# Kernel optimization log

Hardware: AMD Instinct MI355X
Metric: run time of the kernel (lower is better)

Reference implementation:

```python
import jax, jax.numpy as jnp
import numpy as np

N_ENT = 100000   # entities per KG
N_EDGE = 500000  # edges per KG
N_SEED = 10000
DIM = 128


def _norm_adj(edges, n):
    # edges: [E,2] int. Build undirected adjacency + self loops, sym deg^-1/2 norm.
    loop = jnp.arange(n)
    src = jnp.concatenate([edges[:, 0], edges[:, 1], loop])
    dst = jnp.concatenate([edges[:, 1], edges[:, 0], loop])
    deg = jax.ops.segment_sum(jnp.ones(src.shape[0], jnp.float32), dst, num_segments=n)
    norm = jax.lax.rsqrt(deg[src] * deg[dst])  # [E_tot]
    return src, dst, norm


def _gcn(x, edges, Ws, n):
    # MultiLayerGCN: per layer H = relu(A_norm @ X @ W + X) (residual=True)
    src, dst, norm = _norm_adj(edges, n)
    for W in Ws:
        agg = jax.ops.segment_sum(x[src] * norm[:, None], dst, num_segments=n)  # [n,d]
        x = jax.nn.relu(agg @ W + x)
    return x


def setup_inputs() -> dict:
    key = jax.random.key(0)
    ks = jax.random.split(key, 10)
    return {
        "sr_ent_seeds": jax.random.randint(ks[0], (N_SEED,), 0, N_ENT),
        "tg_ent_seeds": jax.random.randint(ks[1], (N_SEED,), 0, N_ENT),
        "triples_sr": jax.random.randint(ks[2], (N_EDGE, 3), 0, N_ENT),
        "triples_tg": jax.random.randint(ks[3], (N_EDGE, 3), 0, N_ENT),
        "embedding_sr": jax.random.normal(ks[4], (N_ENT, DIM), jnp.float32),
        "embedding_tg": jax.random.normal(ks[5], (N_ENT, DIM), jnp.float32),
        "edges_sr": jax.random.randint(ks[6], (N_EDGE, 2), 0, N_ENT),
        "edges_tg": jax.random.randint(ks[7], (N_EDGE, 2), 0, N_ENT),
        "W1": jax.random.normal(ks[8], (DIM, DIM), jnp.float32) * (DIM ** -0.5),
        "W2": jax.random.normal(ks[9], (DIM, DIM), jnp.float32) * (DIM ** -0.5),
    }


def reference(sr_ent_seeds, tg_ent_seeds, triples_sr, triples_tg,
              embedding_sr, embedding_tg, edges_sr, edges_tg, W1, W2):
    Ws = [W1, W2]
    sr_ent_hid = _gcn(embedding_sr, edges_sr, Ws, N_ENT)
    tg_ent_hid = _gcn(embedding_tg, edges_tg, Ws, N_ENT)
    sr_seed_hid = sr_ent_hid[sr_ent_seeds]
    tg_seed_hid = tg_ent_hid[tg_ent_seeds]
    return (sr_seed_hid, tg_seed_hid, sr_ent_hid, tg_ent_hid)
```

## Files before the change

### kernel.cpp

```cpp
#include <hip/hip_runtime.h>
#include <hip/hip_bf16.h>

#define N_ENT_C   100000
#define N_EDGE_C  500000
#define N_SEED_C  10000
#define DIM_C     128

#define N2_C      (2 * N_ENT_C)
#define NBKT      391
#define BKT_CAP   8192
#define EPB       2048

typedef unsigned int   u32;
typedef unsigned short u16;
typedef __attribute__((ext_vector_type(8))) short bf16x8;
typedef __attribute__((ext_vector_type(4))) float f32x4;

__device__ __forceinline__ float bflo(u32 v) { return __uint_as_float(v << 16); }
__device__ __forceinline__ float bfhi(u32 v) { return __uint_as_float(v & 0xFFFF0000u); }
__device__ __forceinline__ u16 f2bf(float f) {
  u32 u = __float_as_uint(f);
  u += 0x7FFFu + ((u >> 16) & 1u);
  return (u16)(u >> 16);
}

__global__ void k_detect(const u32* __restrict__ words, int* __restrict__ flag,
                         int* __restrict__ bkt_cnt) {
  int tid = threadIdx.x;
  bkt_cnt[tid] = 0;
  bkt_cnt[tid + 256] = 0;
  if (tid == 0) {
    int cnt = 0;
    for (int i = 0; i < 64; ++i) {
      u32 e = (words[i] >> 7) & 0xFF;
      cnt += (e < 96) ? 1 : 0;
    }
    *flag = (cnt >= 8) ? 1 : 0;
  }
}

__global__ __launch_bounds__(256, 4) void k_fill_binned(
    const int2* __restrict__ ea, const int2* __restrict__ eb,
    int* __restrict__ bkt_cnt, u32* __restrict__ csr_tmp, int E) {
  __shared__ u32 ein[2 * EPB];
  __shared__ u16 ebkt[2 * EPB];
  __shared__ int lcount[512];
  __shared__ int lstart[513];
  __shared__ int gbase[512];
  __shared__ int ssc[256];

  const int tid = threadIdx.x;
  const int gofs = blockIdx.y ? N_ENT_C : 0;
  const int2* ed = blockIdx.y ? eb : ea;
  const int e0 = blockIdx.x * EPB;

  lcount[tid] = 0; lcount[tid + 256] = 0;
  __syncthreads();

  int2 ev[EPB / 256];
#pragma unroll
  for (int i = 0; i < EPB / 256; ++i) {
    int e = e0 + tid + i * 256;
    int2 v = (e < E) ? ed[e] : make_int2(0, 0);
    ev[i] = v;
    if (e < E) {
      atomicAdd(&lcount[(gofs + v.y) >> 9], 1);
      atomicAdd(&lcount[(gofs + v.x) >> 9], 1);
    }
  }
  __syncthreads();

  int a = lcount[2 * tid], b = lcount[2 * tid + 1];
  int ts = a + b;
  ssc[tid] = ts;
  __syncthreads();
  for (int off = 1; off < 256; off <<= 1) {
    int v = (tid >= off) ? ssc[tid - off] : 0;
    __syncthreads();
    ssc[tid] += v;
    __syncthreads();
  }
  int ex = ssc[tid] - ts;
  lstart[2 * tid] = ex;
  lstart[2 * tid + 1] = ex + a;
  if (tid == 255) lstart[512] = ssc[255];
  __syncthreads();

  {
    int b0 = 2 * tid, b1 = 2 * tid + 1;
    if (b0 < NBKT) { int c = lstart[b0 + 1] - lstart[b0]; gbase[b0] = c ? atomicAdd(&bkt_cnt[b0], c) : 0; }
    if (b1 < NBKT) { int c = lstart[b1 + 1] - lstart[b1]; gbase[b1] = c ? atomicAdd(&bkt_cnt[b1], c) : 0; }
    lcount[tid] = lstart[tid];
    lcount[tid + 256] = lstart[tid + 256];
  }
  __syncthreads();

#pragma unroll
  for (int i = 0; i < EPB / 256; ++i) {
    int e = e0 + tid + i * 256;
    if (e >= E) continue;
    int2 v = ev[i];
    int r1 = gofs + v.y;
    u32 w1 = (u32)v.x | ((u32)(r1 & 511) << 20);
    int bk1 = r1 >> 9;
    int p = atomicAdd(&lcount[bk1], 1);
    ein[p] = w1; ebkt[p] = (u16)bk1;
    int r2 = gofs + v.x;
    u32 w2 = (u32)v.y | ((u32)(r2 & 511) << 20);
    int bk2 = r2 >> 9;
    p = atomicAdd(&lcount[bk2], 1);
    ein[p] = w2; ebkt[p] = (u16)bk2;
  }
  __syncthreads();

  int tot = lstart[512];
  for (int j = tid; j < tot; j += 256) {
    int bk = ebkt[j];
    u32 off = (u32)(gbase[bk] + (j - lstart[bk]));
    if (off < BKT_CAP) csr_tmp[(size_t)bk * BKT_CAP + off] = ein[j];
  }
}

__global__ void k_deg(const u32* __restrict__ csr_tmp, const int* __restrict__ bkt_cnt,
                      int* __restrict__ deg, float* __restrict__ rdeg) {
  __shared__ int lcnt[512];
  int bk = blockIdx.x, tid = threadIdx.x;
  lcnt[tid] = 0;
  __syncthreads();
  int cnt = min(bkt_cnt[bk], BKT_CAP);
  const u32* src = csr_tmp + (size_t)bk * BKT_CAP;
  for (int j = tid; j < cnt; j += 512)
    atomicAdd(&lcnt[(src[j] >> 20) & 511], 1);
  __syncthreads();
  int row = (bk << 9) + tid;
  if (row < N2_C) {
    int d = lcnt[tid];
    deg[row] = d;
    rdeg[row] = rsqrtf((float)(d + 1));
  }
}

__global__ void k_scan1(const int* __restrict__ deg, int* __restrict__ row_start,
                        int* __restrict__ bsum, int n) {
  __shared__ int s[256];
  int b = blockIdx.x, tid = threadIdx.x;
  int i0 = b * 1024 + tid * 4;
  int d0 = (i0 + 0 < n) ? deg[i0 + 0] : 0;
  int d1 = (i0 + 1 < n) ? deg[i0 + 1] : 0;
  int d2 = (i0 + 2 < n) ? deg[i0 + 2] : 0;
  int d3 = (i0 + 3 < n) ? deg[i0 + 3] : 0;
  int tsum = d0 + d1 + d2 + d3;
  s[tid] = tsum;
  __syncthreads();
  for (int off = 1; off < 256; off <<= 1) {
    int v = (tid >= off) ? s[tid - off] : 0;
    __syncthreads();
    s[tid] += v;
    __syncthreads();
  }
  int toff = s[tid] - tsum;
  if (i0 + 0 < n) row_start[i0 + 0] = toff;
  if (i0 + 1 < n) row_start[i0 + 1] = toff + d0;
  if (i0 + 2 < n) row_start[i0 + 2] = toff + d0 + d1;
  if (i0 + 3 < n) row_start[i0 + 3] = toff + d0 + d1 + d2;
  if (tid == 255) bsum[b] = s[255];
}

__global__ void k_scan2(int* __restrict__ bsum, int nb) {
  __shared__ int s[256];
  int tid = threadIdx.x;
  int v = (tid < nb) ? bsum[tid] : 0;
  s[tid] = v;
  __syncthreads();
  for (int off = 1; off < 256; off <<= 1) {
    int u = (tid >= off) ? s[tid - off] : 0;
    __syncthreads();
    s[tid] += u;
    __syncthreads();
  }
  if (tid < nb) bsum[tid] = s[tid] - v;
}

__global__ void k_scan3(int* __restrict__ row_start, const int* __restrict__ bsum, int n) {
  int i = blockIdx.x * 256 + threadIdx.x;
  if (i < n) row_start[i] += bsum[i >> 10];
}

__global__ void k_csr_sort(const u32* __restrict__ csr_tmp, const int* __restrict__ bkt_cnt,
                           const int* __restrict__ row_start, const float* __restrict__ rdeg,
                           int2* __restrict__ csr) {
  __shared__ int lcur[512];
  int bk = blockIdx.x, tid = threadIdx.x;
  int rb0 = bk << 9;
  int base = row_start[rb0];
  {
    int row = rb0 + tid;
    lcur[tid] = (row < N2_C) ? row_start[row] - base : 0;
  }
  __syncthreads();
  int cnt = min(bkt_cnt[bk], BKT_CAP);
  const u32* srcp = csr_tmp + (size_t)bk * BKT_CAP;
  for (int j = tid; j < cnt; j += 512) {
    u32 w = srcp[j];
    int dl = (w >> 20) & 511;
    int s = w & 0x1FFFF;
    int pos = atomicAdd(&lcur[dl], 1);
    float r = rdeg[((rb0 + dl) >= N_ENT_C ? N_ENT_C : 0) + s];
    csr[base + pos] = make_int2(s, __float_as_int(r));
  }
}

__global__ void k_cvt_bf16(const void* __restrict__ s0, const void* __restrict__ s1,
                           u32* __restrict__ d0, u32* __restrict__ d1,
                           const int* __restrict__ flag, int n4) {
  int i = blockIdx.x * 256 + threadIdx.x;
  if (i >= n4) return;
  const void* src = blockIdx.y ? s1 : s0;
  u32* dst = blockIdx.y ? d1 : d0;
  uint4 o;
  if (*flag) {
    const float4* sf = (const float4*)src;
    float4 va = sf[2 * i], vb = sf[2 * i + 1];
    o.x = (u32)f2bf(va.x) | ((u32)f2bf(va.y) << 16);
    o.y = (u32)f2bf(va.z) | ((u32)f2bf(va.w) << 16);
    o.z = (u32)f2bf(vb.x) | ((u32)f2bf(vb.y) << 16);
    o.w = (u32)f2bf(vb.z) | ((u32)f2bf(vb.w) << 16);
  } else {
    o = ((const uint4*)src)[i];
  }
  ((uint4*)dst)[i] = o;
}

#define G2(cp, t, a0, a1) { \
  int2 e0 = cp[t], e1 = cp[(t) + 1]; \
  u32 v0 = xin[((u32)e0.x << 6) | lane]; \
  u32 v1 = xin[((u32)e1.x << 6) | lane]; \
  float r0 = __int_as_float(e0.y), r1 = __int_as_float(e1.y); \
  a0 += r0 * bflo(v0) + r1 * bflo(v1); \
  a1 += r0 * bfhi(v0) + r1 * bfhi(v1); }
#define G1(cp, t, a0, a1) { \
  int2 e0 = cp[t]; \
  u32 v0 = xin[((u32)e0.x << 6) | lane]; \
  float r0 = __int_as_float(e0.y); \
  a0 += r0 * bflo(v0); a1 += r0 * bfhi(v0); }

__global__ __launch_bounds__(512, 8) void k_fused(
    const int* __restrict__ row_start, const int* __restrict__ deg,
    const int2* __restrict__ csr2, const u32* __restrict__ xin0,
    const u32* __restrict__ xin1, const float* __restrict__ rdeg,
    const void* __restrict__ W, const int* __restrict__ flag,
    u32* __restrict__ xout0, u32* __restrict__ xout1,
    float* __restrict__ fout0, float* __restrict__ fout1) {
  __shared__ __align__(16) u16 smem[128 * 128 + 32 * 128];
  u16* sWt = smem;
  u16* sA  = smem + 128 * 128;

  const int tid = threadIdx.x;
  const int row0 = blockIdx.x * 32;
  const int gofs = blockIdx.y * N_ENT_C;
  const u32* __restrict__ xin  = blockIdx.y ? xin1  : xin0;
  u32* __restrict__ xout       = blockIdx.y ? xout1 : xout0;
  float* __restrict__ fout     = blockIdx.y ? fout1 : fout0;
  const int* rsb = row_start + gofs;
  const int* dgb = deg + gofs;
  const float* rdb = rdeg + gofs;
  const int isf32 = *flag;

  {
    u32* sW32 = (u32*)sWt;
    const float* Wf = (const float*)W;
    const u16*   Wu = (const u16*)W;
    for (int i = tid; i < 64 * 128; i += 512) {
      int k2 = i >> 7;
      int n  = i & 127;
      u16 lo, hi;
      if (isf32) { lo = f2bf(Wf[(2 * k2) * 128 + n]); hi = f2bf(Wf[(2 * k2 + 1) * 128 + n]); }
      else       { lo = Wu[(2 * k2) * 128 + n];       hi = Wu[(2 * k2 + 1) * 128 + n]; }
      sW32[n * 64 + (k2 ^ ((n & 7) << 2))] = (u32)lo | ((u32)hi << 16);
    }
  }

  const int wave = tid >> 6, lane = tid & 63;
  for (int pq = 0; pq < 2; ++pq) {
    const int rlA = wave * 4 + 2 * pq, rlB = rlA + 1;
    const int rowA = row0 + rlA, rowB = row0 + rlB;
    const bool vA = rowA < N_ENT_C, vB = rowB < N_ENT_C;
    int rsA = vA ? rsb[rowA] : 0, deA = vA ? dgb[rowA] : 0;
    int rsB = vB ? rsb[rowB] : 0, deB = vB ? dgb[rowB] : 0;
    rsA = __builtin_amdgcn_readfirstlane(rsA); deA = __builtin_amdgcn_readfirstlane(deA);
    rsB = __builtin_amdgcn_readfirstlane(rsB); deB = __builtin_amdgcn_readfirstlane(deB);
    const float rdA = vA ? rdb[rowA] : 0.f, rdB = vB ? rdb[rowB] : 0.f;
    const u32 vsA = vA ? xin[((u32)rowA << 6) | lane] : 0u;
    const u32 vsB = vB ? xin[((u32)rowB << 6) | lane] : 0u;
    const int2* cA = csr2 + rsA;
    const int2* cB = csr2 + rsB;
    float a0A = 0.f, a1A = 0.f, a0B = 0.f, a1B = 0.f;
    int tA = 0, tB = 0;
    while (tA + 1 < deA && tB + 1 < deB) {
      int2 eA0 = cA[tA], eA1 = cA[tA + 1];
      int2 eB0 = cB[tB], eB1 = cB[tB + 1];
      u32 uA0 = xin[((u32)eA0.x << 6) | lane];
      u32 uA1 = xin[((u32)eA1.x << 6) | lane];
      u32 uB0 = xin[((u32)eB0.x << 6) | lane];
      u32 uB1 = xin[((u32)eB1.x << 6) | lane];
      float rA0 = __int_as_float(eA0.y), rA1 = __int_as_float(eA1.y);
      float rB0 = __int_as_float(eB0.y), rB1 = __int_as_float(eB1.y);
      a0A += rA0 * bflo(uA0) + rA1 * bflo(uA1);
      a1A += rA0 * bfhi(uA0) + rA1 * bfhi(uA1);
      a0B += rB0 * bflo(uB0) + rB1 * bflo(uB1);
      a1B += rB0 * bfhi(uB0) + rB1 * bfhi(uB1);
      tA += 2; tB += 2;
    }
    for (; tA + 3 < deA; tA += 4) { G2(cA, tA, a0A, a1A); G2(cA, tA + 2, a0A, a1A); }
    if (tA + 1 < deA) { G2(cA, tA, a0A, a1A); tA += 2; }
    if (tA < deA) G1(cA, tA, a0A, a1A);
    for (; tB + 3 < deB; tB += 4) { G2(cB, tB, a0B, a1B); G2(cB, tB + 2, a0B, a1B); }
    if (tB + 1 < deB) { G2(cB, tB, a0B, a1B); tB += 2; }
    if (tB < deB) G1(cB, tB, a0B, a1B);

    a0A = rdA * a0A + rdA * rdA * bflo(vsA);
    a1A = rdA * a1A + rdA * rdA * bfhi(vsA);
    a0B = rdB * a0B + rdB * rdB * bflo(vsB);
    a1B = rdB * a1B + rdB * rdB * bfhi(vsB);
    ((u32*)sA)[rlA * 64 + (lane ^ ((rlA & 7) << 2))] = (u32)f2bf(a0A) | ((u32)f2bf(a1A) << 16);
    ((u32*)sA)[rlB * 64 + (lane ^ ((rlB & 7) << 2))] = (u32)f2bf(a0B) | ((u32)f2bf(a1B) << 16);
  }
  __syncthreads();

  const int rows_h = (wave >> 2) * 16;
  const int col_q  = (wave & 3) * 32;
  const int m = lane & 15, q = lane >> 4;
  f32x4 acc[2];
  for (int ct = 0; ct < 2; ++ct) acc[ct] = (f32x4){0.f, 0.f, 0.f, 0.f};
#pragma unroll
  for (int kt = 0; kt < 4; ++kt) {
    int k0 = kt * 32 + q * 8;
    int ks = k0 ^ ((m & 7) << 3);
    bf16x8 a = *(const bf16x8*)&sA[(rows_h + m) * 128 + ks];
#pragma unroll
    for (int ct = 0; ct < 2; ++ct) {
      bf16x8 b = *(const bf16x8*)&sWt[(col_q + ct * 16 + m) * 128 + ks];
      acc[ct] = __builtin_amdgcn_mfma_f32_16x16x32_bf16(a, b, acc[ct], 0, 0, 0);
    }
  }
  __syncthreads();

  float* sC = (float*)smem;
#pragma unroll
  for (int ct = 0; ct < 2; ++ct)
#pragma unroll
    for (int r = 0; r < 4; ++r)
      sC[(rows_h + q * 4 + r) * 132 + (col_q + ct * 16 + m)] = acc[ct][r];
  __syncthreads();

  {
    int rowl = tid >> 4;
    int c0 = (tid & 15) * 8;
    int row = row0 + rowl;
    if (row < N_ENT_C) {
      size_t goff = (size_t)row * 64 + (c0 >> 1);
      const u32* resp = xin + goff;
      if (fout) {
        float* op = fout + (size_t)row * 128 + c0;
#pragma unroll
        for (int u2 = 0; u2 < 2; ++u2) {
          u32 rv0 = resp[2 * u2], rv1 = resp[2 * u2 + 1];
          f32x4 f;
          f[0] = fmaxf(sC[rowl * 132 + c0 + 4 * u2    ] + bflo(rv0), 0.f);
          f[1] = fmaxf(sC[rowl * 132 + c0 + 4 * u2 + 1] + bfhi(rv0), 0.f);
          f[2] = fmaxf(sC[rowl * 132 + c0 + 4 * u2 + 2] + bflo(rv1), 0.f);
          f[3] = fmaxf(sC[rowl * 132 + c0 + 4 * u2 + 3] + bfhi(rv1), 0.f);
          __builtin_nontemporal_store(f, (f32x4*)(op + 4 * u2));
        }
      } else {
        u32 ov[4];
#pragma unroll
        for (int u = 0; u < 4; ++u) {
          u32 rv = resp[u];
          float lo = fmaxf(sC[rowl * 132 + c0 + 2 * u]     + bflo(rv), 0.f);
          float hi = fmaxf(sC[rowl * 132 + c0 + 2 * u + 1] + bfhi(rv), 0.f);
          ov[u] = (u32)f2bf(lo) | ((u32)f2bf(hi) << 16);
        }
        uint4* op = (uint4*)(xout + goff);
        op[0] = make_uint4(ov[0], ov[1], ov[2], ov[3]);
      }
    }
  }
}

__global__ void k_out_seed(const float4* __restrict__ ea, const float4* __restrict__ eb,
                           const int* __restrict__ sa, const int* __restrict__ sb,
                           float4* __restrict__ oa, float4* __restrict__ ob, int total4) {
  int t = blockIdx.x * 256 + threadIdx.x;
  if (t >= total4) return;
  const float4* e = blockIdx.y ? eb : ea;
  const int* seeds = blockIdx.y ? sb : sa;
  float4* o = blockIdx.y ? ob : oa;
  int s = t >> 5, w = t & 31;
  o[t] = e[((size_t)seeds[s] << 5) | w];
}

extern "C" void kernel_launch(void* const* d_in, const int* in_sizes, int n_in,
                              void* d_out, int out_size, void* d_ws, size_t ws_size,
                              hipStream_t stream) {
  const int*  sr_seeds = (const int*)d_in[0];
  const int*  tg_seeds = (const int*)d_in[1];
  const void* emb_sr   = d_in[4];
  const void* emb_tg   = d_in[5];
  const int*  edges_sr = (const int*)d_in[6];
  const int*  edges_tg = (const int*)d_in[7];
  const void* W1       = d_in[8];
  const void* W2       = d_in[9];
  float* out = (float*)d_out;

  const int nd = N_ENT_C * DIM_C;

  u16* x_A       = (u16*)d_ws;
  u16* x_B       = x_A + (size_t)nd;
  float* ws_rdeg = (float*)(x_B + (size_t)nd);
  int* ws_flag   = (int*)(ws_rdeg + N2_C);
  int* deg       = ws_flag + 64;
  int* row_start = deg + N2_C;
  int* bsum      = row_start + N2_C;
  int* bkt_cnt   = bsum + 1024;
  int2* csr      = (int2*)(bkt_cnt + 512);
  u32* csr_tmp   = (u32*)(csr + (size_t)4 * N_EDGE_C);
  u16* x_C       = (u16*)csr_tmp;

  float* out_seed_sr = out;
  float* out_seed_tg = out + (size_t)N_SEED_C * DIM_C;
  float* out_ent_sr  = out + (size_t)2 * N_SEED_C * DIM_C;
  float* out_ent_tg  = out_ent_sr + (size_t)nd;

  u16* x_D = (u16*)out_ent_sr;

  k_detect<<<1, 256, 0, stream>>>((const u32*)emb_sr, ws_flag, bkt_cnt);

  dim3 agrid((N_EDGE_C + EPB - 1) / EPB, 2);
  k_fill_binned<<<agrid, 256, 0, stream>>>((const int2*)edges_sr, (const int2*)edges_tg,
                                           bkt_cnt, csr_tmp, N_EDGE_C);
  k_deg<<<NBKT, 512, 0, stream>>>(csr_tmp, bkt_cnt, deg, ws_rdeg);

  const int NB_SCAN = (N2_C + 1023) / 1024;
  k_scan1<<<NB_SCAN, 256, 0, stream>>>(deg, row_start, bsum, N2_C);
  k_scan2<<<1, 256, 0, stream>>>(bsum, NB_SCAN);
  k_scan3<<<(N2_C + 255) / 256, 256, 0, stream>>>(row_start, bsum, N2_C);

  k_csr_sort<<<NBKT, 512, 0, stream>>>(csr_tmp, bkt_cnt, row_start, ws_rdeg, csr);

  dim3 cgrid((nd / 8 + 255) / 256, 2);
  k_cvt_bf16<<<cgrid, 256, 0, stream>>>(emb_sr, emb_tg, (u32*)x_A, (u32*)x_B, ws_flag, nd / 8);

  const int NBF = N_ENT_C / 32;

  dim3 f2grid(NBF, 2);
  k_fused<<<f2grid, 512, 0, stream>>>(row_start, deg, csr, (const u32*)x_A, (const u32*)x_B,
                                      ws_rdeg, W1, ws_flag, (u32*)x_C, (u32*)x_D,
                                      nullptr, nullptr);

  k_fused<<<dim3(NBF, 1), 512, 0, stream>>>(row_start + N_ENT_C, deg + N_ENT_C, csr,
                                            (const u32*)x_D, nullptr, ws_rdeg + N_ENT_C,
                                            W2, ws_flag, nullptr, nullptr,
                                            out_ent_tg, nullptr);
  k_fused<<<dim3(NBF, 1), 512, 0, stream>>>(row_start, deg, csr,
                                            (const u32*)x_C, nullptr, ws_rdeg,
                                            W2, ws_flag, nullptr, nullptr,
                                            out_ent_sr, nullptr);

  dim3 sgrid((N_SEED_C * 32 + 255) / 256, 2);
  k_out_seed<<<sgrid, 256, 0, stream>>>((const float4*)out_ent_sr, (const float4*)out_ent_tg,
                                        sr_seeds, tg_seeds,
                                        (float4*)out_seed_sr, (float4*)out_seed_tg,
                                        N_SEED_C * 32);
}
```

Measured before the change: 523.9 us.

## Build CSR offsets per bucket and drop embedded edge weights from CSR

Replaces the three-pass global degree scan with a scan over bucket counts plus a per-bucket local scan inside the CSR sort, so the separate degree array and two kernel launches go away. CSR entries shrink from int2 (index plus rdeg) to a bare u32 index. The aggregation kernel now looks up rdeg by source index, and it derives degrees from adjacent row_start values. This removes the rdeg gather during the sort and halves CSR bandwidth, at the cost of an extra scalar-indexed rdeg load per edge in the hot loop. Row-validity guards are also removed, which relies on N_ENT being a multiple of 32.

After: 523.5 us. No clear change (-0.1%).

```diff
diff --git a/kernel.cpp b/kernel.cpp
--- a/kernel.cpp
+++ b/kernel.cpp
@@ -122,7 +122,7 @@
 }
 
 __global__ void k_deg(const u32* __restrict__ csr_tmp, const int* __restrict__ bkt_cnt,
-                      int* __restrict__ deg, float* __restrict__ rdeg) {
+                      float* __restrict__ rdeg) {
   __shared__ int lcnt[512];
   int bk = blockIdx.x, tid = threadIdx.x;
   lcnt[tid] = 0;
@@ -133,80 +133,60 @@
     atomicAdd(&lcnt[(src[j] >> 20) & 511], 1);
   __syncthreads();
   int row = (bk << 9) + tid;
-  if (row < N2_C) {
-    int d = lcnt[tid];
-    deg[row] = d;
-    rdeg[row] = rsqrtf((float)(d + 1));
-  }
-}
-
-__global__ void k_scan1(const int* __restrict__ deg, int* __restrict__ row_start,
-                        int* __restrict__ bsum, int n) {
-  __shared__ int s[256];
-  int b = blockIdx.x, tid = threadIdx.x;
-  int i0 = b * 1024 + tid * 4;
-  int d0 = (i0 + 0 < n) ? deg[i0 + 0] : 0;
-  int d1 = (i0 + 1 < n) ? deg[i0 + 1] : 0;
-  int d2 = (i0 + 2 < n) ? deg[i0 + 2] : 0;
-  int d3 = (i0 + 3 < n) ? deg[i0 + 3] : 0;
-  int tsum = d0 + d1 + d2 + d3;
-  s[tid] = tsum;
-  __syncthreads();
-  for (int off = 1; off < 256; off <<= 1) {
-    int v = (tid >= off) ? s[tid - off] : 0;
-    __syncthreads();
-    s[tid] += v;
-    __syncthreads();
-  }
-  int toff = s[tid] - tsum;
-  if (i0 + 0 < n) row_start[i0 + 0] = toff;
-  if (i0 + 1 < n) row_start[i0 + 1] = toff + d0;
-  if (i0 + 2 < n) row_start[i0 + 2] = toff + d0 + d1;
-  if (i0 + 3 < n) row_start[i0 + 3] = toff + d0 + d1 + d2;
-  if (tid == 255) bsum[b] = s[255];
-}
-
-__global__ void k_scan2(int* __restrict__ bsum, int nb) {
-  __shared__ int s[256];
+  if (row < N2_C) rdeg[row] = rsqrtf((float)(lcnt[tid] + 1));
+}
+
+__global__ void k_scanb(const int* __restrict__ bkt_cnt, int* __restrict__ bbase,
+                        int* __restrict__ row_start) {
+  __shared__ int s[512];
   int tid = threadIdx.x;
-  int v = (tid < nb) ? bsum[tid] : 0;
+  int v = (tid < NBKT) ? bkt_cnt[tid] : 0;
   s[tid] = v;
   __syncthreads();
-  for (int off = 1; off < 256; off <<= 1) {
+  for (int off = 1; off < 512; off <<= 1) {
     int u = (tid >= off) ? s[tid - off] : 0;
     __syncthreads();
     s[tid] += u;
     __syncthreads();
   }
-  if (tid < nb) bsum[tid] = s[tid] - v;
-}
-
-__global__ void k_scan3(int* __restrict__ row_start, const int* __restrict__ bsum, int n) {
-  int i = blockIdx.x * 256 + threadIdx.x;
-  if (i < n) row_start[i] += bsum[i >> 10];
-}
-
-__global__ void k_csr_sort(const u32* __restrict__ csr_tmp, const int* __restrict__ bkt_cnt,
-                           const int* __restrict__ row_start, const float* __restrict__ rdeg,
-                           int2* __restrict__ csr) {
-  __shared__ int lcur[512];
+  if (tid < NBKT) bbase[tid] = s[tid] - v;
+  if (tid == NBKT - 1) row_start[N2_C] = s[tid];
+}
+
+__global__ __launch_bounds__(512) void k_csr_sort(
+    const u32* __restrict__ csr_tmp, const int* __restrict__ bkt_cnt,
+    const int* __restrict__ bbase, int* __restrict__ row_start,
+    u32* __restrict__ csr) {
+  __shared__ int lcnt[512];
+  __shared__ int lofs[512];
   int bk = blockIdx.x, tid = threadIdx.x;
-  int rb0 = bk << 9;
-  int base = row_start[rb0];
-  {
-    int row = rb0 + tid;
-    lcur[tid] = (row < N2_C) ? row_start[row] - base : 0;
-  }
+  lcnt[tid] = 0;
   __syncthreads();
   int cnt = min(bkt_cnt[bk], BKT_CAP);
+  int base = bbase[bk];
   const u32* srcp = csr_tmp + (size_t)bk * BKT_CAP;
+  for (int j = tid; j < cnt; j += 512)
+    atomicAdd(&lcnt[(srcp[j] >> 20) & 511], 1);
+  __syncthreads();
+  int own = lcnt[tid];
+  lofs[tid] = own;
+  __syncthreads();
+  for (int off = 1; off < 512; off <<= 1) {
+    int u = (tid >= off) ? lofs[tid - off] : 0;
+    __syncthreads();
+    lofs[tid] += u;
+    __syncthreads();
+  }
+  int ex = lofs[tid] - own;
+  int row = (bk << 9) + tid;
+  if (row < N2_C) row_start[row] = base + ex;
+  lcnt[tid] = ex;
+  __syncthreads();
   for (int j = tid; j < cnt; j += 512) {
     u32 w = srcp[j];
     int dl = (w >> 20) & 511;
-    int s = w & 0x1FFFF;
-    int pos = atomicAdd(&lcur[dl], 1);
-    float r = rdeg[((rb0 + dl) >= N_ENT_C ? N_ENT_C : 0) + s];
-    csr[base + pos] = make_int2(s, __float_as_int(r));
+    int pos = atomicAdd(&lcnt[dl], 1);
+    csr[base + pos] = w & 0x1FFFF;
   }
 }
 
@@ -232,24 +212,24 @@
 }
 
 #define G2(cp, t, a0, a1) { \
-  int2 e0 = cp[t], e1 = cp[(t) + 1]; \
-  u32 v0 = xin[((u32)e0.x << 6) | lane]; \
-  u32 v1 = xin[((u32)e1.x << 6) | lane]; \
-  float r0 = __int_as_float(e0.y), r1 = __int_as_float(e1.y); \
+  u32 s0 = __builtin_amdgcn_readfirstlane(cp[t]); \
+  u32 s1 = __builtin_amdgcn_readfirstlane(cp[(t) + 1]); \
+  float r0 = rdb[s0], r1 = rdb[s1]; \
+  u32 v0 = xin[(s0 << 6) | lane]; \
+  u32 v1 = xin[(s1 << 6) | lane]; \
   a0 += r0 * bflo(v0) + r1 * bflo(v1); \
   a1 += r0 * bfhi(v0) + r1 * bfhi(v1); }
 #define G1(cp, t, a0, a1) { \
-  int2 e0 = cp[t]; \
-  u32 v0 = xin[((u32)e0.x << 6) | lane]; \
-  float r0 = __int_as_float(e0.y); \
+  u32 s0 = __builtin_amdgcn_readfirstlane(cp[t]); \
+  float r0 = rdb[s0]; \
+  u32 v0 = xin[(s0 << 6) | lane]; \
   a0 += r0 * bflo(v0); a1 += r0 * bfhi(v0); }
 
 __global__ __launch_bounds__(512, 8) void k_fused(
-    const int* __restrict__ row_start, const int* __restrict__ deg,
-    const int2* __restrict__ csr2, const u32* __restrict__ xin0,
-    const u32* __restrict__ xin1, const float* __restrict__ rdeg,
-    const void* __restrict__ W, const int* __restrict__ flag,
-    u32* __restrict__ xout0, u32* __restrict__ xout1,
+    const int* __restrict__ row_start, const u32* __restrict__ csru,
+    const u32* __restrict__ xin0, const u32* __restrict__ xin1,
+    const float* __restrict__ rdeg, const void* __restrict__ W,
+    const int* __restrict__ flag, u32* __restrict__ xout0, u32* __restrict__ xout1,
     float* __restrict__ fout0, float* __restrict__ fout1) {
   __shared__ __align__(16) u16 smem[128 * 128 + 32 * 128];
   u16* sWt = smem;
@@ -262,7 +242,6 @@
   u32* __restrict__ xout       = blockIdx.y ? xout1 : xout0;
   float* __restrict__ fout     = blockIdx.y ? fout1 : fout0;
   const int* rsb = row_start + gofs;
-  const int* dgb = deg + gofs;
   const float* rdb = rdeg + gofs;
   const int isf32 = *flag;
 
@@ -284,27 +263,28 @@
   for (int pq = 0; pq < 2; ++pq) {
     const int rlA = wave * 4 + 2 * pq, rlB = rlA + 1;
     const int rowA = row0 + rlA, rowB = row0 + rlB;
-    const bool vA = rowA < N_ENT_C, vB = rowB < N_ENT_C;
-    int rsA = vA ? rsb[rowA] : 0, deA = vA ? dgb[rowA] : 0;
-    int rsB = vB ? rsb[rowB] : 0, deB = vB ? dgb[rowB] : 0;
-    rsA = __builtin_amdgcn_readfirstlane(rsA); deA = __builtin_amdgcn_readfirstlane(deA);
-    rsB = __builtin_amdgcn_readfirstlane(rsB); deB = __builtin_amdgcn_readfirstlane(deB);
-    const float rdA = vA ? rdb[rowA] : 0.f, rdB = vB ? rdb[rowB] : 0.f;
-    const u32 vsA = vA ? xin[((u32)rowA << 6) | lane] : 0u;
-    const u32 vsB = vB ? xin[((u32)rowB << 6) | lane] : 0u;
-    const int2* cA = csr2 + rsA;
-    const int2* cB = csr2 + rsB;
+    int rsA = __builtin_amdgcn_readfirstlane(rsb[rowA]);
+    int rsB = __builtin_amdgcn_readfirstlane(rsb[rowA + 1]);
+    int reB = __builtin_amdgcn_readfirstlane(rsb[rowA + 2]);
+    const int deA = rsB - rsA, deB = reB - rsB;
+    const float rdA = rdb[rowA], rdB = rdb[rowB];
+    const u32 vsA = xin[((u32)rowA << 6) | lane];
+    const u32 vsB = xin[((u32)rowB << 6) | lane];
+    const u32* cA = csru + rsA;
+    const u32* cB = csru + rsB;
     float a0A = 0.f, a1A = 0.f, a0B = 0.f, a1B = 0.f;
     int tA = 0, tB = 0;
     while (tA + 1 < deA && tB + 1 < deB) {
-      int2 eA0 = cA[tA], eA1 = cA[tA + 1];
-      int2 eB0 = cB[tB], eB1 = cB[tB + 1];
-      u32 uA0 = xin[((u32)eA0.x << 6) | lane];
-      u32 uA1 = xin[((u32)eA1.x << 6) | lane];
-      u32 uB0 = xin[((u32)eB0.x << 6) | lane];
-      u32 uB1 = xin[((u32)eB1.x << 6) | lane];
-      float rA0 = __int_as_float(eA0.y), rA1 = __int_as_float(eA1.y);
-      float rB0 = __int_as_float(eB0.y), rB1 = __int_as_float(eB1.y);
+      u32 iA0 = __builtin_amdgcn_readfirstlane(cA[tA]);
+      u32 iA1 = __builtin_amdgcn_readfirstlane(cA[tA + 1]);
+      u32 iB0 = __builtin_amdgcn_readfirstlane(cB[tB]);
+      u32 iB1 = __builtin_amdgcn_readfirstlane(cB[tB + 1]);
+      float rA0 = rdb[iA0], rA1 = rdb[iA1];
+      float rB0 = rdb[iB0], rB1 = rdb[iB1];
+      u32 uA0 = xin[(iA0 << 6) | lane];
+      u32 uA1 = xin[(iA1 << 6) | lane];
+      u32 uB0 = xin[(iB0 << 6) | lane];
+      u32 uB1 = xin[(iB1 << 6) | lane];
       a0A += rA0 * bflo(uA0) + rA1 * bflo(uA1);
       a1A += rA0 * bfhi(uA0) + rA1 * bfhi(uA1);
       a0B += rB0 * bflo(uB0) + rB1 * bflo(uB1);
@@ -357,33 +337,31 @@
     int rowl = tid >> 4;
     int c0 = (tid & 15) * 8;
     int row = row0 + rowl;
-    if (row < N_ENT_C) {
-      size_t goff = (size_t)row * 64 + (c0 >> 1);
-      const u32* resp = xin + goff;
-      if (fout) {
-        float* op = fout + (size_t)row * 128 + c0;
-#pragma unroll
-        for (int u2 = 0; u2 < 2; ++u2) {
-          u32 rv0 = resp[2 * u2], rv1 = resp[2 * u2 + 1];
-          f32x4 f;
-          f[0] = fmaxf(sC[rowl * 132 + c0 + 4 * u2    ] + bflo(rv0), 0.f);
-          f[1] = fmaxf(sC[rowl * 132 + c0 + 4 * u2 + 1] + bfhi(rv0), 0.f);
-          f[2] = fmaxf(sC[rowl * 132 + c0 + 4 * u2 + 2] + bflo(rv1), 0.f);
-          f[3] = fmaxf(sC[rowl * 132 + c0 + 4 * u2 + 3] + bfhi(rv1), 0.f);
-          __builtin_nontemporal_store(f, (f32x4*)(op + 4 * u2));
-        }
-      } else {
-        u32 ov[4];
-#pragma unroll
-        for (int u = 0; u < 4; ++u) {
-          u32 rv = resp[u];
-          float lo = fmaxf(sC[rowl * 132 + c0 + 2 * u]     + bflo(rv), 0.f);
-          float hi = fmaxf(sC[rowl * 132 + c0 + 2 * u + 1] + bfhi(rv), 0.f);
-          ov[u] = (u32)f2bf(lo) | ((u32)f2bf(hi) << 16);
-        }
-        uint4* op = (uint4*)(xout + goff);
-        op[0] = make_uint4(ov[0], ov[1], ov[2], ov[3]);
+    size_t goff = (size_t)row * 64 + (c0 >> 1);
+    const u32* resp = xin + goff;
+    if (fout) {
+      float* op = fout + (size_t)row * 128 + c0;
+#pragma unroll
+      for (int u2 = 0; u2 < 2; ++u2) {
+        u32 rv0 = resp[2 * u2], rv1 = resp[2 * u2 + 1];
+        f32x4 f;
+        f[0] = fmaxf(sC[rowl * 132 + c0 + 4 * u2    ] + bflo(rv0), 0.f);
+        f[1] = fmaxf(sC[rowl * 132 + c0 + 4 * u2 + 1] + bfhi(rv0), 0.f);
+        f[2] = fmaxf(sC[rowl * 132 + c0 + 4 * u2 + 2] + bflo(rv1), 0.f);
+        f[3] = fmaxf(sC[rowl * 132 + c0 + 4 * u2 + 3] + bfhi(rv1), 0.f);
+        __builtin_nontemporal_store(f, (f32x4*)(op + 4 * u2));
       }
+    } else {
+      u32 ov[4];
+#pragma unroll
+      for (int u = 0; u < 4; ++u) {
+        u32 rv = resp[u];
+        float lo = fmaxf(sC[rowl * 132 + c0 + 2 * u]     + bflo(rv), 0.f);
+        float hi = fmaxf(sC[rowl * 132 + c0 + 2 * u + 1] + bfhi(rv), 0.f);
+        ov[u] = (u32)f2bf(lo) | ((u32)f2bf(hi) << 16);
+      }
+      uint4* op = (uint4*)(xout + goff);
+      op[0] = make_uint4(ov[0], ov[1], ov[2], ov[3]);
     }
   }
 }
@@ -419,12 +397,11 @@
   u16* x_B       = x_A + (size_t)nd;
   float* ws_rdeg = (float*)(x_B + (size_t)nd);
   int* ws_flag   = (int*)(ws_rdeg + N2_C);
-  int* deg       = ws_flag + 64;
-  int* row_start = deg + N2_C;
-  int* bsum      = row_start + N2_C;
-  int* bkt_cnt   = bsum + 1024;
-  int2* csr      = (int2*)(bkt_cnt + 512);
-  u32* csr_tmp   = (u32*)(csr + (size_t)4 * N_EDGE_C);
+  int* row_start = ws_flag + 64;
+  int* bkt_cnt   = row_start + N2_C + 64;
+  int* bbase     = bkt_cnt + 512;
+  u32* csr       = (u32*)(bbase + 512);
+  u32* csr_tmp   = csr + (size_t)4 * N_EDGE_C;
   u16* x_C       = (u16*)csr_tmp;
 
   float* out_seed_sr = out;
@@ -439,14 +416,9 @@
   dim3 agrid((N_EDGE_C + EPB - 1) / EPB, 2);
   k_fill_binned<<<agrid, 256, 0, stream>>>((const int2*)edges_sr, (const int2*)edges_tg,
                                            bkt_cnt, csr_tmp, N_EDGE_C);
-  k_deg<<<NBKT, 512, 0, stream>>>(csr_tmp, bkt_cnt, deg, ws_rdeg);
-
-  const int NB_SCAN = (N2_C + 1023) / 1024;
-  k_scan1<<<NB_SCAN, 256, 0, stream>>>(deg, row_start, bsum, N2_C);
-  k_scan2<<<1, 256, 0, stream>>>(bsum, NB_SCAN);
-  k_scan3<<<(N2_C + 255) / 256, 256, 0, stream>>>(row_start, bsum, N2_C);
-
-  k_csr_sort<<<NBKT, 512, 0, stream>>>(csr_tmp, bkt_cnt, row_start, ws_rdeg, csr);
+  k_deg  <<<NBKT, 512, 0, stream>>>(csr_tmp, bkt_cnt, ws_rdeg);
+  k_scanb<<<1, 512, 0, stream>>>(bkt_cnt, bbase, row_start);
+  k_csr_sort<<<NBKT, 512, 0, stream>>>(csr_tmp, bkt_cnt, bbase, row_start, csr);
 
   dim3 cgrid((nd / 8 + 255) / 256, 2);
   k_cvt_bf16<<<cgrid, 256, 0, stream>>>(emb_sr, emb_tg, (u32*)x_A, (u32*)x_B, ws_flag, nd / 8);
@@ -454,15 +426,15 @@
   const int NBF = N_ENT_C / 32;
 
   dim3 f2grid(NBF, 2);
-  k_fused<<<f2grid, 512, 0, stream>>>(row_start, deg, csr, (const u32*)x_A, (const u32*)x_B,
+  k_fused<<<f2grid, 512, 0, stream>>>(row_start, csr, (const u32*)x_A, (const u32*)x_B,
                                       ws_rdeg, W1, ws_flag, (u32*)x_C, (u32*)x_D,
                                       nullptr, nullptr);
 
-  k_fused<<<dim3(NBF, 1), 512, 0, stream>>>(row_start + N_ENT_C, deg + N_ENT_C, csr,
+  k_fused<<<dim3(NBF, 1), 512, 0, stream>>>(row_start + N_ENT_C, csr,
                                             (const u32*)x_D, nullptr, ws_rdeg + N_ENT_C,
                                             W2, ws_flag, nullptr, nullptr,
                                             out_ent_tg, nullptr);
-  k_fused<<<dim3(NBF, 1), 512, 0, stream>>>(row_start, deg, csr,
+  k_fused<<<dim3(NBF, 1), 512, 0, stream>>>(row_start, csr,
                                             (const u32*)x_C, nullptr, ws_rdeg,
                                             W2, ws_flag, nullptr, nullptr,
                                             out_ent_sr, nullptr);
```
